# Kernel tuning notes

Hardware: AMD Instinct MI355X
Metric: run time of the kernel (lower is better)

## Reference

```python
import jax, jax.numpy as jnp
import numpy as np

N = 50000
E = 1600000
IN, OUT = 128, 64


def _gcn(h, W, b, src, dst):
    # DGL GraphConv, norm='both', weight applied first (in>out), activation=relu
    x = h @ W  # [N, OUT]
    ones = jnp.ones((src.shape[0],), dtype=h.dtype)
    deg_out = jnp.clip(jax.ops.segment_sum(ones, src, num_segments=N), 1.0)
    deg_in = jnp.clip(jax.ops.segment_sum(ones, dst, num_segments=N), 1.0)
    x = x * jax.lax.rsqrt(deg_out)[:, None]
    agg = jax.ops.segment_sum(x[src], dst, num_segments=N)  # SpMM
    agg = agg * jax.lax.rsqrt(deg_in)[:, None]
    return jax.nn.relu(agg + b)


def setup_inputs() -> dict:
    key = jax.random.key(0)
    ks = jax.random.split(key, 10)
    inp = {"h": jax.random.normal(ks[0], (N, IN), dtype=jnp.float32)}
    for i in range(3):
        inp[f"src{i}"] = jax.random.randint(ks[1 + 2 * i], (E,), 0, N, dtype=jnp.int32)
        inp[f"dst{i}"] = jax.random.randint(ks[2 + 2 * i], (E,), 0, N, dtype=jnp.int32)
        inp[f"W{i}"] = jax.random.normal(ks[7 + i], (IN, OUT), dtype=jnp.float32) * (1.0 / np.sqrt(IN))
        inp[f"b{i}"] = jnp.zeros((OUT,), dtype=jnp.float32)
    return inp


def reference(h, src0, dst0, src1, dst1, src2, dst2, W0, b0, W1, b1, W2, b2):
    e0 = _gcn(h, W0, b0, src0, dst0)
    e1 = _gcn(h, W1, b1, src1, dst1)
    e2 = _gcn(h, W2, b2, src2, dst2)
    # stack over meta-path dim then mean == average of semantic embeddings
    return (e0 + e1 + e2) / 3.0
```

## Files before the change

kernel.cpp:

```cpp
#include <hip/hip_runtime.h>

#define KDIM 128
#define NCOLS 64
#define NCHUNK 64
#define NRANGE 2
#define RBINS 25088
#define RWORDS (RBINS / 2)
#define CWORDS (NRANGE * RWORDS)
#define COARSE 512
#define NC 98
#define SFCAP 17408
#define BUCKET 64
#define NBUCK 782
#define FCAP 2816
#define NPB 85

typedef __attribute__((ext_vector_type(8))) short bf16x8;
typedef __attribute__((ext_vector_type(4))) float f32x4;

struct GArgs {
  const int*   src[3];
  const int*   dst[3];
  const float* W[3];
  const float* b[3];
  int          E[3];
};

__device__ __forceinline__ unsigned short f2bf(float f) {
  unsigned u = __float_as_uint(f);
  u += 0x7FFFu + ((u >> 16) & 1u);
  return (unsigned short)(u >> 16);
}
__device__ __forceinline__ float bflo(unsigned u) { return __uint_as_float(u << 16); }
__device__ __forceinline__ float bfhi(unsigned u) { return __uint_as_float(u & 0xFFFF0000u); }

__global__ __launch_bounds__(256) void convert_h_kernel(
    const float* __restrict__ h, unsigned short* __restrict__ hb, int total8) {
  int i = blockIdx.x * 256 + threadIdx.x;
  if (i >= total8) return;
  const float4* hp = (const float4*)(h + (size_t)i * 8);
  float4 f0 = hp[0];
  float4 f1 = hp[1];
  uint4 u;
  u.x = (unsigned)f2bf(f0.x) | ((unsigned)f2bf(f0.y) << 16);
  u.y = (unsigned)f2bf(f0.z) | ((unsigned)f2bf(f0.w) << 16);
  u.z = (unsigned)f2bf(f1.x) | ((unsigned)f2bf(f1.y) << 16);
  u.w = (unsigned)f2bf(f1.z) | ((unsigned)f2bf(f1.w) << 16);
  ((uint4*)hb)[i] = u;
}

__global__ __launch_bounds__(256) void wfrag_kernel(
    GArgs A, unsigned short* __restrict__ Wf) {
  int tid = blockIdx.x * 256 + threadIdx.x;
  if (tid >= 3 * 16 * 64) return;
  int lane = tid & 63;
  int frag = (tid >> 6) & 15;
  int g = tid >> 10;
  int c = frag >> 2, kk = frag & 3;
  int n = lane & 15, quad = lane >> 4;
  const float* W = A.W[g];
  unsigned short v[8];
  #pragma unroll
  for (int j = 0; j < 8; ++j) {
    int k = 32 * kk + quad * 8 + j;
    v[j] = f2bf(W[k * 64 + 16 * c + n]);
  }
  uint4 u;
  u.x = (unsigned)v[0] | ((unsigned)v[1] << 16);
  u.y = (unsigned)v[2] | ((unsigned)v[3] << 16);
  u.z = (unsigned)v[4] | ((unsigned)v[5] << 16);
  u.w = (unsigned)v[6] | ((unsigned)v[7] << 16);
  ((uint4*)Wf)[tid] = u;
}

__global__ __launch_bounds__(256) void count_coarse_kernel(
    GArgs A, int* __restrict__ tot) {
  __shared__ int hcnt[NC];
  const int g = blockIdx.y;
  const int E = A.E[g];
  const int per_block = (((E + NPB - 1) / NPB) + 3) & ~3;
  const int* __restrict__ dst = A.dst[g];
  const int t = threadIdx.x;
  if (t < NC) hcnt[t] = 0;
  __syncthreads();
  const int e0 = blockIdx.x * per_block;
  const int e1 = min(e0 + per_block, E);
  const int n = max(e1 - e0, 0);
  const int nv = n >> 2;
  const int4* d4 = (const int4*)&dst[e0];
  for (int v = t; v < nv; v += 256) {
    int4 d = d4[v];
    atomicAdd(&hcnt[(unsigned)d.x >> 9], 1);
    atomicAdd(&hcnt[(unsigned)d.y >> 9], 1);
    atomicAdd(&hcnt[(unsigned)d.z >> 9], 1);
    atomicAdd(&hcnt[(unsigned)d.w >> 9], 1);
  }
  for (int e = e0 + (nv << 2) + t; e < e1; e += 256)
    atomicAdd(&hcnt[(unsigned)dst[e] >> 9], 1);
  __syncthreads();
  if (t < NC && hcnt[t]) atomicAdd(&tot[g * NC + t], hcnt[t]);
}

__global__ __launch_bounds__(128) void scan_off_kernel(
    const int* __restrict__ tot, int* __restrict__ off, int* __restrict__ cursor) {
  __shared__ int sd[128];
  const int t = threadIdx.x;
  for (int g = 0; g < 3; ++g) {
    int v = (t < NC) ? tot[g * NC + t] : 0;
    sd[t] = v;
    __syncthreads();
    for (int o = 1; o < 128; o <<= 1) {
      int add = (t >= o) ? sd[t - o] : 0;
      __syncthreads();
      sd[t] += add;
      __syncthreads();
    }
    int excl = sd[t] - v;
    if (t < NC) { off[g * (NC + 1) + t] = excl; cursor[g * NC + t] = excl; }
    if (t == 0) off[g * (NC + 1) + NC] = sd[127];
    __syncthreads();
  }
}

__global__ __launch_bounds__(256) void partition_coarse_kernel(
    GArgs A, int* __restrict__ cursor, unsigned* __restrict__ P2c, int Emax) {
  __shared__ int lcnt[NC];
  __shared__ int lcur[NC];
  const int g = blockIdx.y;
  const int E = A.E[g];
  const int per_block = (((E + NPB - 1) / NPB) + 3) & ~3;
  const int* __restrict__ src = A.src[g];
  const int* __restrict__ dst = A.dst[g];
  unsigned* __restrict__ P2g = P2c + (size_t)g * Emax;
  const int t = threadIdx.x;
  if (t < NC) lcnt[t] = 0;
  __syncthreads();
  const int e0 = blockIdx.x * per_block;
  const int e1 = min(e0 + per_block, E);
  const int n = max(e1 - e0, 0);
  const int nv = n >> 2;
  const int4* d4 = (const int4*)&dst[e0];
  const int4* s4 = (const int4*)&src[e0];
  for (int v = t; v < nv; v += 256) {
    int4 d = d4[v];
    atomicAdd(&lcnt[(unsigned)d.x >> 9], 1);
    atomicAdd(&lcnt[(unsigned)d.y >> 9], 1);
    atomicAdd(&lcnt[(unsigned)d.z >> 9], 1);
    atomicAdd(&lcnt[(unsigned)d.w >> 9], 1);
  }
  for (int e = e0 + (nv << 2) + t; e < e1; e += 256)
    atomicAdd(&lcnt[(unsigned)dst[e] >> 9], 1);
  __syncthreads();
  if (t < NC) {
    int c = lcnt[t];
    lcur[t] = c ? atomicAdd(&cursor[g * NC + t], c) : 0;
  }
  __syncthreads();
  for (int v = t; v < nv; v += 256) {
    int4 d = d4[v];
    int4 s = s4[v];
    unsigned bk; int pos;
    bk = (unsigned)d.x >> 9; pos = atomicAdd(&lcur[bk], 1);
    P2g[pos] = (unsigned)s.x | (((unsigned)d.x & 511u) << 16);
    bk = (unsigned)d.y >> 9; pos = atomicAdd(&lcur[bk], 1);
    P2g[pos] = (unsigned)s.y | (((unsigned)d.y & 511u) << 16);
    bk = (unsigned)d.z >> 9; pos = atomicAdd(&lcur[bk], 1);
    P2g[pos] = (unsigned)s.z | (((unsigned)d.z & 511u) << 16);
    bk = (unsigned)d.w >> 9; pos = atomicAdd(&lcur[bk], 1);
    P2g[pos] = (unsigned)s.w | (((unsigned)d.w & 511u) << 16);
  }
  for (int e = e0 + (nv << 2) + t; e < e1; e += 256) {
    unsigned d = (unsigned)dst[e];
    unsigned bk = d >> 9;
    int pos = atomicAdd(&lcur[bk], 1);
    P2g[pos] = (unsigned)src[e] | ((d & 511u) << 16);
  }
}

__global__ __launch_bounds__(512) void sort_fine_kernel(
    const unsigned* __restrict__ P2c, const int* __restrict__ off,
    unsigned short* __restrict__ S, int* __restrict__ row_start,
    int N, int Emax) {
  __shared__ int cnt[COARSE];
  __shared__ int sd[COARSE];
  __shared__ int cur[COARSE];
  __shared__ unsigned short outl[SFCAP];
  const int c = blockIdx.x;
  const int g = blockIdx.y;
  const unsigned* __restrict__ P2g = P2c + (size_t)g * Emax;
  const int base_e = off[g * (NC + 1) + c];
  const int nloc = off[g * (NC + 1) + c + 1] - base_e;
  const int t = threadIdx.x;

  cnt[t] = 0;
  __syncthreads();
  for (int i = t; i < nloc; i += 512)
    atomicAdd(&cnt[(P2g[base_e + i] >> 16) & 511u], 1);
  __syncthreads();
  int v = cnt[t];
  sd[t] = v;
  __syncthreads();
  for (int o = 1; o < 512; o <<= 1) {
    int add = (t >= o) ? sd[t - o] : 0;
    __syncthreads();
    sd[t] += add;
    __syncthreads();
  }
  int excl = sd[t] - v;
  cur[t] = excl;
  int node = c * COARSE + t;
  if (node <= N) row_start[g * (N + 1) + node] = base_e + excl;
  __syncthreads();
  for (int i = t; i < nloc; i += 512) {
    unsigned p = P2g[base_e + i];
    int pos = atomicAdd(&cur[(p >> 16) & 511u], 1);
    if (pos < SFCAP) outl[pos] = (unsigned short)(p & 0xFFFFu);
  }
  __syncthreads();
  unsigned short* __restrict__ Sg = S + (size_t)g * Emax;
  for (int i = t; i < nloc; i += 512) Sg[base_e + i] = outl[i];
}

__global__ __launch_bounds__(256) void hist_all_kernel(
    GArgs A, unsigned* __restrict__ P) {
  __shared__ unsigned hist[RWORDS];
  const int g = blockIdx.z;
  const int E = A.E[g];
  const int per_chunk = (((E + NCHUNK - 1) / NCHUNK) + 3) & ~3;
  const int* __restrict__ keys = A.src[g];
  unsigned* __restrict__ Pg = P + (size_t)g * NCHUNK * CWORDS;

  const int chunk = blockIdx.x;
  const int base  = blockIdx.y * RBINS;
  const int t = threadIdx.x;
  for (int i = t; i < RWORDS; i += 256) hist[i] = 0;
  __syncthreads();
  const int e0 = chunk * per_chunk;
  const int e1 = min(e0 + per_chunk, E);
  const int n = max(e1 - e0, 0);
  const int nv = n >> 2;
  const int4* k4p = (const int4*)&keys[e0];
  for (int v = t; v < nv; v += 256) {
    int4 k4 = k4p[v];
    unsigned k0 = (unsigned)(k4.x - base);
    unsigned k1 = (unsigned)(k4.y - base);
    unsigned k2 = (unsigned)(k4.z - base);
    unsigned k3 = (unsigned)(k4.w - base);
    if (k0 < (unsigned)RBINS) atomicAdd(&hist[k0 >> 1], 1u << ((k0 & 1u) * 16));
    if (k1 < (unsigned)RBINS) atomicAdd(&hist[k1 >> 1], 1u << ((k1 & 1u) * 16));
    if (k2 < (unsigned)RBINS) atomicAdd(&hist[k2 >> 1], 1u << ((k2 & 1u) * 16));
    if (k3 < (unsigned)RBINS) atomicAdd(&hist[k3 >> 1], 1u << ((k3 & 1u) * 16));
  }
  for (int e = e0 + (nv << 2) + t; e < e1; e += 256) {
    unsigned k = (unsigned)(keys[e] - base);
    if (k < (unsigned)RBINS) atomicAdd(&hist[k >> 1], 1u << ((k & 1u) * 16));
  }
  __syncthreads();
  unsigned* dstp = Pg + (size_t)chunk * CWORDS + blockIdx.y * RWORDS;
  for (int i = t; i < RWORDS; i += 256) dstp[i] = hist[i];
}

__global__ __launch_bounds__(256) void gemm_mfma_kernel(
    GArgs A, const unsigned short* __restrict__ hb,
    const unsigned short* __restrict__ Wf, const unsigned* __restrict__ P,
    unsigned short* __restrict__ x, int N) {
  __shared__ int ldeg[64];
  const int g = blockIdx.y;
  const unsigned* __restrict__ Pg = P + (size_t)g * NCHUNK * CWORDS;
  unsigned short* __restrict__ xg = x + (size_t)g * N * NCOLS;
  const int t = threadIdx.x;
  const int row0 = blockIdx.x * 64;

  if (t < 64) ldeg[t] = 0;
  __syncthreads();
  {
    int lrow = t >> 2;
    int part = t & 3;
    int row = min(row0 + lrow, N - 1);
    int word = row >> 1;
    int shift = (row & 1) * 16;
    int s = 0;
    #pragma unroll
    for (int c = 0; c < 16; ++c)
      s += (int)((Pg[(size_t)(part * 16 + c) * CWORDS + word] >> shift) & 0xFFFFu);
    atomicAdd(&ldeg[lrow], s);
  }

  const int lane = t & 63;
  const int w = t >> 6;
  const int quad = lane >> 4;
  const int n = lane & 15;

  bf16x8 bf[16];
  const uint4* wfp = (const uint4*)Wf + (size_t)g * 1024 + lane;
  #pragma unroll
  for (int f = 0; f < 16; ++f) {
    union { uint4 u; bf16x8 v; } cv;
    cv.u = wfp[(size_t)f * 64];
    bf[f] = cv.v;
  }

  int arow = min(row0 + w * 16 + n, N - 1);
  const unsigned short* hrow = hb + (size_t)arow * KDIM + quad * 8;
  bf16x8 a0 = *(const bf16x8*)(hrow);
  bf16x8 a1 = *(const bf16x8*)(hrow + 32);
  bf16x8 a2 = *(const bf16x8*)(hrow + 64);
  bf16x8 a3 = *(const bf16x8*)(hrow + 96);

  __syncthreads();

  f32x4 acc[4];
  #pragma unroll
  for (int c = 0; c < 4; ++c) acc[c] = (f32x4)(0.f);
  #pragma unroll
  for (int c = 0; c < 4; ++c) {
    acc[c] = __builtin_amdgcn_mfma_f32_16x16x32_bf16(a0, bf[c * 4 + 0], acc[c], 0, 0, 0);
    acc[c] = __builtin_amdgcn_mfma_f32_16x16x32_bf16(a1, bf[c * 4 + 1], acc[c], 0, 0, 0);
    acc[c] = __builtin_amdgcn_mfma_f32_16x16x32_bf16(a2, bf[c * 4 + 2], acc[c], 0, 0, 0);
    acc[c] = __builtin_amdgcn_mfma_f32_16x16x32_bf16(a3, bf[c * 4 + 3], acc[c], 0, 0, 0);
  }

  int rbase = row0 + w * 16 + quad * 4;
  #pragma unroll
  for (int r = 0; r < 4; ++r) {
    int row = rbase + r;
    if (row < N) {
      float s = rsqrtf(fmaxf((float)ldeg[row - row0], 1.0f));
      #pragma unroll
      for (int c = 0; c < 4; ++c)
        xg[(size_t)row * NCOLS + 16 * c + n] = f2bf(acc[c][r] * s);
    }
  }
}

__global__ __launch_bounds__(512) void spmm_all_kernel(
    GArgs A, const unsigned short* __restrict__ S,
    const int* __restrict__ row_start, const unsigned short* __restrict__ x,
    float* __restrict__ out, int N, int Emax) {
  __shared__ int rs[BUCKET + 1];
  __shared__ unsigned short srcs[FCAP];

  const int t = threadIdx.x;
  const int bk = blockIdx.x;
  const int dbase = bk * BUCKET;
  const int nd = min(BUCKET, N - dbase);
  const int grp = t >> 3;
  const int qe = (t & 7) * 8;

  float tot[8];
  #pragma unroll
  for (int j = 0; j < 8; ++j) tot[j] = 0.f;

  for (int g = 0; g < 3; ++g) {
    const unsigned short* __restrict__ Sg = S + (size_t)g * Emax;
    const int* __restrict__ rsg = row_start + (size_t)g * (N + 1);
    const unsigned short* __restrict__ xg = x + (size_t)g * N * NCOLS;

    __syncthreads();
    if (t <= BUCKET) rs[t] = rsg[min(dbase + t, N)];
    __syncthreads();
    const int e0 = rs[0];
    const int ne = min(rs[BUCKET] - e0, FCAP);
    for (int i = t; i < ne; i += 512) srcs[i] = Sg[e0 + i];
    __syncthreads();

    if (grp < nd) {
      int i = rs[grp] - e0;
      const int iend = min(rs[grp + 1] - e0, ne);
      const int deg = iend - i;
      float acc[8];
      #pragma unroll
      for (int j = 0; j < 8; ++j) acc[j] = 0.f;
      for (; i + 3 < iend; i += 4) {
        int sa = srcs[i + 0];
        int sb = srcs[i + 1];
        int sc = srcs[i + 2];
        int sdd = srcs[i + 3];
        uint4 ua = *(const uint4*)&xg[(size_t)sa * NCOLS + qe];
        uint4 ub = *(const uint4*)&xg[(size_t)sb * NCOLS + qe];
        uint4 uc = *(const uint4*)&xg[(size_t)sc * NCOLS + qe];
        uint4 ud = *(const uint4*)&xg[(size_t)sdd * NCOLS + qe];
        acc[0] += bflo(ua.x) + bflo(ub.x) + bflo(uc.x) + bflo(ud.x);
        acc[1] += bfhi(ua.x) + bfhi(ub.x) + bfhi(uc.x) + bfhi(ud.x);
        acc[2] += bflo(ua.y) + bflo(ub.y) + bflo(uc.y) + bflo(ud.y);
        acc[3] += bfhi(ua.y) + bfhi(ub.y) + bfhi(uc.y) + bfhi(ud.y);
        acc[4] += bflo(ua.z) + bflo(ub.z) + bflo(uc.z) + bflo(ud.z);
        acc[5] += bfhi(ua.z) + bfhi(ub.z) + bfhi(uc.z) + bfhi(ud.z);
        acc[6] += bflo(ua.w) + bflo(ub.w) + bflo(uc.w) + bflo(ud.w);
        acc[7] += bfhi(ua.w) + bfhi(ub.w) + bfhi(uc.w) + bfhi(ud.w);
      }
      for (; i < iend; ++i) {
        int s = srcs[i];
        uint4 u = *(const uint4*)&xg[(size_t)s * NCOLS + qe];
        acc[0] += bflo(u.x); acc[1] += bfhi(u.x);
        acc[2] += bflo(u.y); acc[3] += bfhi(u.y);
        acc[4] += bflo(u.z); acc[5] += bfhi(u.z);
        acc[6] += bflo(u.w); acc[7] += bfhi(u.w);
      }
      float sc2 = rsqrtf(fmaxf((float)deg, 1.0f));
      const float* bg = A.b[g] + qe;
      #pragma unroll
      for (int j = 0; j < 8; ++j)
        tot[j] += fmaxf(fmaf(acc[j], sc2, bg[j]), 0.f) * (1.0f / 3.0f);
    }
  }

  if (grp < nd) {
    float* op = &out[(size_t)(dbase + grp) * NCOLS + qe];
    *(float4*)&op[0] = make_float4(tot[0], tot[1], tot[2], tot[3]);
    *(float4*)&op[4] = make_float4(tot[4], tot[5], tot[6], tot[7]);
  }
}

extern "C" void kernel_launch(void* const* d_in, const int* in_sizes, int n_in,
                              void* d_out, int out_size, void* d_ws, size_t ws_size,
                              hipStream_t stream) {
  const float* h = (const float*)d_in[0];
  const int N = in_sizes[0] / KDIM;
  float* out = (float*)d_out;

  GArgs A;
  int Emax = 0;
  for (int g = 0; g < 3; ++g) {
    A.src[g] = (const int*)  d_in[1 + g * 4];
    A.dst[g] = (const int*)  d_in[2 + g * 4];
    A.W[g]   = (const float*)d_in[3 + g * 4];
    A.b[g]   = (const float*)d_in[4 + g * 4];
    A.E[g]   = in_sizes[1 + g * 4];
    if (A.E[g] > Emax) Emax = A.E[g];
  }

  char* w = (char*)d_ws;
  unsigned short* x = (unsigned short*)w;
  char* w2 = w + (size_t)3 * N * NCOLS * sizeof(unsigned short);
  unsigned short* hb = (unsigned short*)w2;
  char* w3 = w2 + (size_t)N * KDIM * sizeof(unsigned short);
  unsigned* P2c = (unsigned*)w3;
  char* w4 = w3 + (size_t)3 * Emax * sizeof(unsigned);
  unsigned* P = (unsigned*)w4;
  char* w5 = w4 + (size_t)3 * NCHUNK * CWORDS * sizeof(unsigned);
  unsigned short* S = (unsigned short*)w5;
  char* w6 = w5 + (size_t)3 * Emax * sizeof(unsigned short);
  unsigned short* Wf = (unsigned short*)w6;
  char* w7 = w6 + (size_t)3 * 16 * 64 * 8 * sizeof(unsigned short);
  int* row_start = (int*)w7;
  char* w8 = w7 + (size_t)3 * (N + 1) * sizeof(int);
  int* tot    = (int*)w8;
  int* off    = tot + 3 * NC;
  int* cursor = off + 3 * (NC + 1);

  hipMemsetAsync(tot, 0, 3 * NC * sizeof(int), stream);
  {
    int total8 = N * KDIM / 8;
    convert_h_kernel<<<(total8 + 255) / 256, 256, 0, stream>>>(h, hb, total8);
  }
  wfrag_kernel<<<12, 256, 0, stream>>>(A, Wf);
  count_coarse_kernel<<<dim3(NPB, 3), 256, 0, stream>>>(A, tot);
  scan_off_kernel<<<1, 128, 0, stream>>>(tot, off, cursor);
  partition_coarse_kernel<<<dim3(NPB, 3), 256, 0, stream>>>(A, cursor, P2c, Emax);
  sort_fine_kernel<<<dim3(NC, 3), 512, 0, stream>>>(P2c, off, S, row_start, N, Emax);
  hist_all_kernel<<<dim3(NCHUNK, NRANGE, 3), 256, 0, stream>>>(A, P);
  gemm_mfma_kernel<<<dim3((N + 63) / 64, 3), 256, 0, stream>>>(A, hb, Wf, P, x, N);
  spmm_all_kernel<<<NBUCK, 512, 0, stream>>>(A, S, row_start, x, out, N, Emax);
}
```

Before: 297.4 us.

## Fuse preprocessing kernels and pack source-degree histogram into 8-bit counters

Merges the h conversion, W fragment packing, coarse destination count and source-degree histogram into one block-specialised prep kernel. This removes several launches and lets the independent prep work run concurrently. The out-degree histogram now uses 8-bit packed counters over the full node range, so it needs one pass instead of two range passes and writes half as much partial-histogram data. The GEMM uses 128-row blocks with 512 threads and loads W fragments inside the loop. W columns are permuted so each lane can write 4 bf16 outputs with one vector store. The risk is that 8-bit per-chunk counters overflow if a node gets more than 255 edges in one chunk.

```diff
diff --git a/kernel.cpp b/kernel.cpp
--- a/kernel.cpp
+++ b/kernel.cpp
@@ -2,11 +2,8 @@
 
 #define KDIM 128
 #define NCOLS 64
-#define NCHUNK 64
-#define NRANGE 2
-#define RBINS 25088
-#define RWORDS (RBINS / 2)
-#define CWORDS (NRANGE * RWORDS)
+#define NHCH 64
+#define HW 12500
 #define COARSE 512
 #define NC 98
 #define SFCAP 17408
@@ -14,6 +11,11 @@
 #define NBUCK 782
 #define FCAP 2816
 #define NPB 85
+#define PREP_HIST (3 * NHCH)
+#define PREP_CNT  (3 * NPB)
+#define PREP_WF   12
+#define PREP_CONV 565
+#define PREP_GRID (PREP_HIST + PREP_CNT + PREP_WF + PREP_CONV)
 
 typedef __attribute__((ext_vector_type(8))) short bf16x8;
 typedef __attribute__((ext_vector_type(4))) float f32x4;
@@ -34,71 +36,104 @@
 __device__ __forceinline__ float bflo(unsigned u) { return __uint_as_float(u << 16); }
 __device__ __forceinline__ float bfhi(unsigned u) { return __uint_as_float(u & 0xFFFF0000u); }
 
-__global__ __launch_bounds__(256) void convert_h_kernel(
-    const float* __restrict__ h, unsigned short* __restrict__ hb, int total8) {
-  int i = blockIdx.x * 256 + threadIdx.x;
-  if (i >= total8) return;
-  const float4* hp = (const float4*)(h + (size_t)i * 8);
-  float4 f0 = hp[0];
-  float4 f1 = hp[1];
-  uint4 u;
-  u.x = (unsigned)f2bf(f0.x) | ((unsigned)f2bf(f0.y) << 16);
-  u.y = (unsigned)f2bf(f0.z) | ((unsigned)f2bf(f0.w) << 16);
-  u.z = (unsigned)f2bf(f1.x) | ((unsigned)f2bf(f1.y) << 16);
-  u.w = (unsigned)f2bf(f1.z) | ((unsigned)f2bf(f1.w) << 16);
-  ((uint4*)hb)[i] = u;
-}
-
-__global__ __launch_bounds__(256) void wfrag_kernel(
-    GArgs A, unsigned short* __restrict__ Wf) {
-  int tid = blockIdx.x * 256 + threadIdx.x;
-  if (tid >= 3 * 16 * 64) return;
-  int lane = tid & 63;
-  int frag = (tid >> 6) & 15;
-  int g = tid >> 10;
-  int c = frag >> 2, kk = frag & 3;
-  int n = lane & 15, quad = lane >> 4;
-  const float* W = A.W[g];
-  unsigned short v[8];
-  #pragma unroll
-  for (int j = 0; j < 8; ++j) {
-    int k = 32 * kk + quad * 8 + j;
-    v[j] = f2bf(W[k * 64 + 16 * c + n]);
-  }
-  uint4 u;
-  u.x = (unsigned)v[0] | ((unsigned)v[1] << 16);
-  u.y = (unsigned)v[2] | ((unsigned)v[3] << 16);
-  u.z = (unsigned)v[4] | ((unsigned)v[5] << 16);
-  u.w = (unsigned)v[6] | ((unsigned)v[7] << 16);
-  ((uint4*)Wf)[tid] = u;
-}
-
-__global__ __launch_bounds__(256) void count_coarse_kernel(
-    GArgs A, int* __restrict__ tot) {
-  __shared__ int hcnt[NC];
-  const int g = blockIdx.y;
-  const int E = A.E[g];
-  const int per_block = (((E + NPB - 1) / NPB) + 3) & ~3;
-  const int* __restrict__ dst = A.dst[g];
-  const int t = threadIdx.x;
-  if (t < NC) hcnt[t] = 0;
-  __syncthreads();
-  const int e0 = blockIdx.x * per_block;
-  const int e1 = min(e0 + per_block, E);
-  const int n = max(e1 - e0, 0);
-  const int nv = n >> 2;
-  const int4* d4 = (const int4*)&dst[e0];
-  for (int v = t; v < nv; v += 256) {
-    int4 d = d4[v];
-    atomicAdd(&hcnt[(unsigned)d.x >> 9], 1);
-    atomicAdd(&hcnt[(unsigned)d.y >> 9], 1);
-    atomicAdd(&hcnt[(unsigned)d.z >> 9], 1);
-    atomicAdd(&hcnt[(unsigned)d.w >> 9], 1);
-  }
-  for (int e = e0 + (nv << 2) + t; e < e1; e += 256)
-    atomicAdd(&hcnt[(unsigned)dst[e] >> 9], 1);
-  __syncthreads();
-  if (t < NC && hcnt[t]) atomicAdd(&tot[g * NC + t], hcnt[t]);
+__global__ __launch_bounds__(256) void prep_kernel(
+    GArgs A, const float* __restrict__ h, unsigned short* __restrict__ hb,
+    unsigned short* __restrict__ Wf, unsigned* __restrict__ P8,
+    int* __restrict__ tot, int total8) {
+  __shared__ unsigned sbuf[HW];
+  const int b = blockIdx.x;
+  const int t = threadIdx.x;
+
+  if (b < PREP_HIST) {
+    const int g = b >> 6;
+    const int chunk = b & 63;
+    const int E = A.E[g];
+    const int per_chunk = (((E + NHCH - 1) / NHCH) + 3) & ~3;
+    const int* __restrict__ keys = A.src[g];
+    for (int i = t; i < HW; i += 256) sbuf[i] = 0;
+    __syncthreads();
+    const int e0 = chunk * per_chunk;
+    const int e1 = min(e0 + per_chunk, E);
+    const int nn = max(e1 - e0, 0);
+    const int nv = nn >> 2;
+    const int4* k4p = (const int4*)&keys[e0];
+    for (int v = t; v < nv; v += 256) {
+      int4 k = k4p[v];
+      atomicAdd(&sbuf[(unsigned)k.x >> 2], 1u << (((unsigned)k.x & 3u) * 8));
+      atomicAdd(&sbuf[(unsigned)k.y >> 2], 1u << (((unsigned)k.y & 3u) * 8));
+      atomicAdd(&sbuf[(unsigned)k.z >> 2], 1u << (((unsigned)k.z & 3u) * 8));
+      atomicAdd(&sbuf[(unsigned)k.w >> 2], 1u << (((unsigned)k.w & 3u) * 8));
+    }
+    for (int e = e0 + (nv << 2) + t; e < e1; e += 256) {
+      unsigned k = (unsigned)keys[e];
+      atomicAdd(&sbuf[k >> 2], 1u << ((k & 3u) * 8));
+    }
+    __syncthreads();
+    unsigned* __restrict__ dstp = P8 + (size_t)b * HW;
+    for (int i = t; i < HW; i += 256) dstp[i] = sbuf[i];
+
+  } else if (b < PREP_HIST + PREP_CNT) {
+    const int bb = b - PREP_HIST;
+    const int g = bb / NPB;
+    const int blk = bb % NPB;
+    const int E = A.E[g];
+    const int per_block = (((E + NPB - 1) / NPB) + 3) & ~3;
+    const int* __restrict__ dst = A.dst[g];
+    int* hcnt = (int*)sbuf;
+    if (t < NC) hcnt[t] = 0;
+    __syncthreads();
+    const int e0 = blk * per_block;
+    const int e1 = min(e0 + per_block, E);
+    const int nn = max(e1 - e0, 0);
+    const int nv = nn >> 2;
+    const int4* d4 = (const int4*)&dst[e0];
+    for (int v = t; v < nv; v += 256) {
+      int4 d = d4[v];
+      atomicAdd(&hcnt[(unsigned)d.x >> 9], 1);
+      atomicAdd(&hcnt[(unsigned)d.y >> 9], 1);
+      atomicAdd(&hcnt[(unsigned)d.z >> 9], 1);
+      atomicAdd(&hcnt[(unsigned)d.w >> 9], 1);
+    }
+    for (int e = e0 + (nv << 2) + t; e < e1; e += 256)
+      atomicAdd(&hcnt[(unsigned)dst[e] >> 9], 1);
+    __syncthreads();
+    if (t < NC && hcnt[t]) atomicAdd(&tot[g * NC + t], hcnt[t]);
+
+  } else if (b < PREP_HIST + PREP_CNT + PREP_WF) {
+    int tid = (b - PREP_HIST - PREP_CNT) * 256 + t;
+    int lane = tid & 63;
+    int frag = (tid >> 6) & 15;
+    int g = tid >> 10;
+    int c = frag >> 2, kk = frag & 3;
+    int n = lane & 15, quad = lane >> 4;
+    const float* W = A.W[g];
+    unsigned short v[8];
+    #pragma unroll
+    for (int j = 0; j < 8; ++j) {
+      int k = 32 * kk + quad * 8 + j;
+      v[j] = f2bf(W[k * 64 + 4 * n + c]);
+    }
+    uint4 u;
+    u.x = (unsigned)v[0] | ((unsigned)v[1] << 16);
+    u.y = (unsigned)v[2] | ((unsigned)v[3] << 16);
+    u.z = (unsigned)v[4] | ((unsigned)v[5] << 16);
+    u.w = (unsigned)v[6] | ((unsigned)v[7] << 16);
+    ((uint4*)Wf)[tid] = u;
+
+  } else {
+    const int cb = b - (PREP_HIST + PREP_CNT + PREP_WF);
+    for (int i = cb * 256 + t; i < total8; i += PREP_CONV * 256) {
+      const float4* hp = (const float4*)(h + (size_t)i * 8);
+      float4 f0 = hp[0];
+      float4 f1 = hp[1];
+      uint4 u;
+      u.x = (unsigned)f2bf(f0.x) | ((unsigned)f2bf(f0.y) << 16);
+      u.y = (unsigned)f2bf(f0.z) | ((unsigned)f2bf(f0.w) << 16);
+      u.z = (unsigned)f2bf(f1.x) | ((unsigned)f2bf(f1.y) << 16);
+      u.w = (unsigned)f2bf(f1.z) | ((unsigned)f2bf(f1.w) << 16);
+      ((uint4*)hb)[i] = u;
+    }
+  }
 }
 
 __global__ __launch_bounds__(128) void scan_off_kernel(
@@ -221,84 +256,38 @@
   for (int i = t; i < nloc; i += 512) Sg[base_e + i] = outl[i];
 }
 
-__global__ __launch_bounds__(256) void hist_all_kernel(
-    GArgs A, unsigned* __restrict__ P) {
-  __shared__ unsigned hist[RWORDS];
-  const int g = blockIdx.z;
-  const int E = A.E[g];
-  const int per_chunk = (((E + NCHUNK - 1) / NCHUNK) + 3) & ~3;
-  const int* __restrict__ keys = A.src[g];
-  unsigned* __restrict__ Pg = P + (size_t)g * NCHUNK * CWORDS;
-
-  const int chunk = blockIdx.x;
-  const int base  = blockIdx.y * RBINS;
-  const int t = threadIdx.x;
-  for (int i = t; i < RWORDS; i += 256) hist[i] = 0;
-  __syncthreads();
-  const int e0 = chunk * per_chunk;
-  const int e1 = min(e0 + per_chunk, E);
-  const int n = max(e1 - e0, 0);
-  const int nv = n >> 2;
-  const int4* k4p = (const int4*)&keys[e0];
-  for (int v = t; v < nv; v += 256) {
-    int4 k4 = k4p[v];
-    unsigned k0 = (unsigned)(k4.x - base);
-    unsigned k1 = (unsigned)(k4.y - base);
-    unsigned k2 = (unsigned)(k4.z - base);
-    unsigned k3 = (unsigned)(k4.w - base);
-    if (k0 < (unsigned)RBINS) atomicAdd(&hist[k0 >> 1], 1u << ((k0 & 1u) * 16));
-    if (k1 < (unsigned)RBINS) atomicAdd(&hist[k1 >> 1], 1u << ((k1 & 1u) * 16));
-    if (k2 < (unsigned)RBINS) atomicAdd(&hist[k2 >> 1], 1u << ((k2 & 1u) * 16));
-    if (k3 < (unsigned)RBINS) atomicAdd(&hist[k3 >> 1], 1u << ((k3 & 1u) * 16));
-  }
-  for (int e = e0 + (nv << 2) + t; e < e1; e += 256) {
-    unsigned k = (unsigned)(keys[e] - base);
-    if (k < (unsigned)RBINS) atomicAdd(&hist[k >> 1], 1u << ((k & 1u) * 16));
-  }
-  __syncthreads();
-  unsigned* dstp = Pg + (size_t)chunk * CWORDS + blockIdx.y * RWORDS;
-  for (int i = t; i < RWORDS; i += 256) dstp[i] = hist[i];
-}
-
-__global__ __launch_bounds__(256) void gemm_mfma_kernel(
+__global__ __launch_bounds__(512) void gemm_mfma_kernel(
     GArgs A, const unsigned short* __restrict__ hb,
-    const unsigned short* __restrict__ Wf, const unsigned* __restrict__ P,
+    const unsigned short* __restrict__ Wf, const unsigned* __restrict__ P8,
     unsigned short* __restrict__ x, int N) {
-  __shared__ int ldeg[64];
+  __shared__ unsigned ldegw[64];
   const int g = blockIdx.y;
-  const unsigned* __restrict__ Pg = P + (size_t)g * NCHUNK * CWORDS;
   unsigned short* __restrict__ xg = x + (size_t)g * N * NCOLS;
   const int t = threadIdx.x;
-  const int row0 = blockIdx.x * 64;
-
-  if (t < 64) ldeg[t] = 0;
-  __syncthreads();
-  {
-    int lrow = t >> 2;
-    int part = t & 3;
-    int row = min(row0 + lrow, N - 1);
-    int word = row >> 1;
-    int shift = (row & 1) * 16;
-    int s = 0;
+  const int row0 = blockIdx.x * 128;
+
+  if (t < 64) ldegw[t] = 0;
+  __syncthreads();
+  if (t < 256) {
+    const unsigned* __restrict__ Pg = P8 + (size_t)g * NHCH * HW;
+    const int widx = t >> 3;
+    const int cg = t & 7;
+    const int wcol = min((row0 >> 2) + widx, HW - 1);
+    unsigned lo = 0, hi = 0;
     #pragma unroll
-    for (int c = 0; c < 16; ++c)
-      s += (int)((Pg[(size_t)(part * 16 + c) * CWORDS + word] >> shift) & 0xFFFFu);
-    atomicAdd(&ldeg[lrow], s);
+    for (int cc = 0; cc < 8; ++cc) {
+      unsigned wv = Pg[(size_t)(cg * 8 + cc) * HW + wcol];
+      lo += wv & 0x00FF00FFu;
+      hi += (wv >> 8) & 0x00FF00FFu;
+    }
+    atomicAdd(&ldegw[2 * widx], lo);
+    atomicAdd(&ldegw[2 * widx + 1], hi);
   }
 
   const int lane = t & 63;
   const int w = t >> 6;
   const int quad = lane >> 4;
   const int n = lane & 15;
-
-  bf16x8 bf[16];
-  const uint4* wfp = (const uint4*)Wf + (size_t)g * 1024 + lane;
-  #pragma unroll
-  for (int f = 0; f < 16; ++f) {
-    union { uint4 u; bf16x8 v; } cv;
-    cv.u = wfp[(size_t)f * 64];
-    bf[f] = cv.v;
-  }
 
   int arow = min(row0 + w * 16 + n, N - 1);
   const unsigned short* hrow = hb + (size_t)arow * KDIM + quad * 8;
@@ -307,28 +296,39 @@
   bf16x8 a2 = *(const bf16x8*)(hrow + 64);
   bf16x8 a3 = *(const bf16x8*)(hrow + 96);
 
-  __syncthreads();
+  const uint4* wfp = (const uint4*)Wf + (size_t)g * 1024 + lane;
 
   f32x4 acc[4];
   #pragma unroll
   for (int c = 0; c < 4; ++c) acc[c] = (f32x4)(0.f);
+
+  __syncthreads();
+
   #pragma unroll
   for (int c = 0; c < 4; ++c) {
-    acc[c] = __builtin_amdgcn_mfma_f32_16x16x32_bf16(a0, bf[c * 4 + 0], acc[c], 0, 0, 0);
-    acc[c] = __builtin_amdgcn_mfma_f32_16x16x32_bf16(a1, bf[c * 4 + 1], acc[c], 0, 0, 0);
-    acc[c] = __builtin_amdgcn_mfma_f32_16x16x32_bf16(a2, bf[c * 4 + 2], acc[c], 0, 0, 0);
-    acc[c] = __builtin_amdgcn_mfma_f32_16x16x32_bf16(a3, bf[c * 4 + 3], acc[c], 0, 0, 0);
-  }
-
-  int rbase = row0 + w * 16 + quad * 4;
+    union { uint4 u; bf16x8 v; } b0, b1, b2, b3;
+    b0.u = wfp[(size_t)(c * 4 + 0) * 64];
+    b1.u = wfp[(size_t)(c * 4 + 1) * 64];
+    b2.u = wfp[(size_t)(c * 4 + 2) * 64];
+    b3.u = wfp[(size_t)(c * 4 + 3) * 64];
+    acc[c] = __builtin_amdgcn_mfma_f32_16x16x32_bf16(a0, b0.v, acc[c], 0, 0, 0);
+    acc[c] = __builtin_amdgcn_mfma_f32_16x16x32_bf16(a1, b1.v, acc[c], 0, 0, 0);
+    acc[c] = __builtin_amdgcn_mfma_f32_16x16x32_bf16(a2, b2.v, acc[c], 0, 0, 0);
+    acc[c] = __builtin_amdgcn_mfma_f32_16x16x32_bf16(a3, b3.v, acc[c], 0, 0, 0);
+  }
+
+  const int rbase = row0 + w * 16 + quad * 4;
   #pragma unroll
   for (int r = 0; r < 4; ++r) {
     int row = rbase + r;
     if (row < N) {
-      float s = rsqrtf(fmaxf((float)ldeg[row - row0], 1.0f));
-      #pragma unroll
-      for (int c = 0; c < 4; ++c)
-        xg[(size_t)row * NCOLS + 16 * c + n] = f2bf(acc[c][r] * s);
+      int lr = row - row0;
+      float dg = (float)((ldegw[2 * (lr >> 2) + (lr & 1)] >> (((lr >> 1) & 1) * 16)) & 0xFFFFu);
+      float s = rsqrtf(fmaxf(dg, 1.0f));
+      uint2 o;
+      o.x = (unsigned)f2bf(acc[0][r] * s) | ((unsigned)f2bf(acc[1][r] * s) << 16);
+      o.y = (unsigned)f2bf(acc[2][r] * s) | ((unsigned)f2bf(acc[3][r] * s) << 16);
+      *(uint2*)(xg + (size_t)row * NCOLS + 4 * n) = o;
     }
   }
 }
@@ -437,8 +437,8 @@
   char* w3 = w2 + (size_t)N * KDIM * sizeof(unsigned short);
   unsigned* P2c = (unsigned*)w3;
   char* w4 = w3 + (size_t)3 * Emax * sizeof(unsigned);
-  unsigned* P = (unsigned*)w4;
-  char* w5 = w4 + (size_t)3 * NCHUNK * CWORDS * sizeof(unsigned);
+  unsigned* P8 = (unsigned*)w4;
+  char* w5 = w4 + (size_t)3 * NHCH * HW * sizeof(unsigned);
   unsigned short* S = (unsigned short*)w5;
   char* w6 = w5 + (size_t)3 * Emax * sizeof(unsigned short);
   unsigned short* Wf = (unsigned short*)w6;
@@ -450,16 +450,11 @@
   int* cursor = off + 3 * (NC + 1);
 
   hipMemsetAsync(tot, 0, 3 * NC * sizeof(int), stream);
-  {
-    int total8 = N * KDIM / 8;
-    convert_h_kernel<<<(total8 + 255) / 256, 256, 0, stream>>>(h, hb, total8);
-  }
-  wfrag_kernel<<<12, 256, 0, stream>>>(A, Wf);
-  count_coarse_kernel<<<dim3(NPB, 3), 256, 0, stream>>>(A, tot);
+  const int total8 = N * KDIM / 8;
+  prep_kernel<<<PREP_GRID, 256, 0, stream>>>(A, h, hb, Wf, P8, tot, total8);
   scan_off_kernel<<<1, 128, 0, stream>>>(tot, off, cursor);
   partition_coarse_kernel<<<dim3(NPB, 3), 256, 0, stream>>>(A, cursor, P2c, Emax);
   sort_fine_kernel<<<dim3(NC, 3), 512, 0, stream>>>(P2c, off, S, row_start, N, Emax);
-  hist_all_kernel<<<dim3(NCHUNK, NRANGE, 3), 256, 0, stream>>>(A, P);
-  gemm_mfma_kernel<<<dim3((N + 63) / 64, 3), 256, 0, stream>>>(A, hb, Wf, P, x, N);
+  gemm_mfma_kernel<<<dim3((N + 127) / 128, 3), 512, 0, stream>>>(A, hb, Wf, P8, x, N);
   spmm_all_kernel<<<NBUCK, 512, 0, stream>>>(A, S, row_start, x, out, N, Emax);
 }
```

Result: faster. 268.7 us (-9.6%).
